# Kernel optimization log

Hardware: AMD Instinct MI355X
Metric: run time of the kernel (lower is better)

The kernel has to match this reference:

```python
import jax, jax.numpy as jnp
import numpy as np

B, L, DIM = 8, 2048, 768
EXPAND, D_STATE, D_CONV = 2, 16, 4
D_INNER = EXPAND * DIM           # 1536
DT_RANK = (DIM + 15) // 16       # 48
EPS = 1e-5


def setup_inputs() -> dict:
    key = jax.random.key(0)
    ks = jax.random.split(key, 8)
    s = lambda k, shape, scale=0.02: jax.random.normal(k, shape, jnp.float32) * scale
    x = jax.random.normal(ks[0], (B, L, DIM), jnp.float32)
    mask = jax.random.randint(ks[1], (B, L), 0, 2).astype(jnp.int32)
    return {
        "x": x,
        "mask": mask,
        "ln_g": jnp.ones((DIM,), jnp.float32),
        "ln_b": jnp.zeros((DIM,), jnp.float32),
        "W_in": s(ks[2], (2 * D_INNER, DIM)),
        "conv_w": s(ks[3], (D_INNER, 1, D_CONV), 0.1),
        "conv_b": jnp.zeros((D_INNER,), jnp.float32),
        "W_xp": s(ks[4], (DT_RANK + 2 * D_STATE, D_INNER)),
        "W_dt": s(ks[5], (D_INNER, DT_RANK), 0.1),
        "b_dt": jnp.full((D_INNER,), -4.6, jnp.float32),  # softplus(b) ~ 0.01 (standard dt init)
        "A_log": jnp.log(jnp.broadcast_to(jnp.arange(1.0, D_STATE + 1.0, dtype=jnp.float32), (D_INNER, D_STATE))),
        "Dp": jnp.ones((D_INNER,), jnp.float32),
        "W_out": s(ks[6], (DIM, D_INNER)),
    }


def _mamba(xn, W_in, conv_w, conv_b, W_xp, W_dt, b_dt, A_log, Dp, W_out):
    # in_proj then split into ssm branch and gate z
    xz = xn @ W_in.T                             # (B, L, 2*D_INNER)
    x_in, z = jnp.split(xz, 2, axis=-1)
    # depthwise causal conv1d + SiLU
    xc = jax.lax.conv_general_dilated(
        jnp.transpose(x_in, (0, 2, 1)), conv_w,
        window_strides=(1,), padding=[(D_CONV - 1, 0)],
        feature_group_count=D_INNER)             # (B, D_INNER, L)
    xc = jnp.transpose(jax.nn.silu(xc + conv_b[None, :, None]), (0, 2, 1))  # (B, L, D_INNER)
    # input-dependent dt, B, C
    xdbl = xc @ W_xp.T                           # (B, L, DT_RANK + 2*D_STATE)
    dt_in, Bm, Cm = jnp.split(xdbl, [DT_RANK, DT_RANK + D_STATE], axis=-1)
    dt = jax.nn.softplus(dt_in @ W_dt.T + b_dt)  # (B, L, D_INNER)
    A = -jnp.exp(A_log)                          # (D_INNER, D_STATE)

    def step(h, inp):
        dt_t, B_t, C_t, x_t = inp                # (B,D_INNER) (B,D_STATE) (B,D_STATE) (B,D_INNER)
        h = jnp.exp(dt_t[:, :, None] * A) * h + (dt_t * x_t)[:, :, None] * B_t[:, None, :]
        y = jnp.einsum('bds,bs->bd', h, C_t)
        return h, y

    h0 = jnp.zeros((B, D_INNER, D_STATE), xn.dtype)
    tm = lambda a: jnp.swapaxes(a, 0, 1)         # time-major for scan
    _, ys = jax.lax.scan(step, h0, (tm(dt), tm(Bm), tm(Cm), tm(xc)))
    y = jnp.swapaxes(ys, 0, 1) + xc * Dp         # skip term D*x
    y = y * jax.nn.silu(z)                       # gate
    return y @ W_out.T


def reference(x, mask, ln_g, ln_b, W_in, conv_w, conv_b, W_xp, W_dt, b_dt, A_log, Dp, W_out):
    mf = mask[..., None].astype(x.dtype)         # (B, L, 1)
    residual = x * mf
    mu = jnp.mean(x, -1, keepdims=True)
    var = jnp.mean((x - mu) ** 2, -1, keepdims=True)
    xn = (x - mu) * jax.lax.rsqrt(var + EPS) * ln_g + ln_b
    xn = xn * mf
    y = _mamba(xn, W_in, conv_w, conv_b, W_xp, W_dt, b_dt, A_log, Dp, W_out)
    # dropout is identity in eval mode
    return residual + y * mf
```

## Files before the change

kernel.cpp:

```cpp
#include <hip/hip_runtime.h>
#include <math.h>

#define Bn 8
#define Ln 2048
#define DIMn 768
#define DIN 1536
#define DSTATE 16
#define DTRANK 48
#define XPN 80
#define NR (Bn*Ln)
#define CH 128
#define NCH (Ln/CH)
#define NDG 6

typedef unsigned short bf16_t;
typedef __attribute__((ext_vector_type(8))) short short8;
typedef __attribute__((ext_vector_type(4))) float f32x4;
typedef __attribute__((ext_vector_type(4))) unsigned short u16x4;

__device__ __forceinline__ float sigf(float v){
    float e = __builtin_amdgcn_exp2f(v * -1.44269504f);
    return __builtin_amdgcn_rcpf(1.0f + e);
}
__device__ __forceinline__ float bf2f(unsigned short u){
    return __uint_as_float(((unsigned int)u) << 16);
}
__device__ __forceinline__ unsigned short f2bf(float f){
    unsigned int x = __float_as_uint(f);
    unsigned int r = (x + 0x7FFFu + ((x >> 16) & 1u)) >> 16;
    return (unsigned short)r;
}

__device__ __forceinline__ void async_ld16(const bf16_t* g, bf16_t* l) {
    __builtin_amdgcn_global_load_lds(
        (const __attribute__((address_space(1))) unsigned int*)g,
        (__attribute__((address_space(3))) unsigned int*)l,
        16, 0, 0);
}

#define ASM_BAR()   __builtin_amdgcn_s_barrier()
#define ASM_VM(N)   asm volatile("s_waitcnt vmcnt(" #N ")" ::: "memory")

__global__ __launch_bounds__(256) void f2bf_kernel(
    const float* __restrict__ in, bf16_t* __restrict__ out, int n)
{
    int i = blockIdx.x*256 + threadIdx.x;
    if (i < n) out[i] = f2bf(in[i]);
}
__global__ __launch_bounds__(256) void padxp_kernel(
    const float* __restrict__ W, bf16_t* __restrict__ out)
{
    int i = blockIdx.x*256 + threadIdx.x;
    int row = i / DIN, col = i % DIN;
    out[i] = (row < XPN) ? f2bf(W[row*DIN + col]) : 0;
}
__global__ __launch_bounds__(256) void paddt_kernel(
    const float* __restrict__ W, bf16_t* __restrict__ out)
{
    int i = blockIdx.x*256 + threadIdx.x;
    int row = i >> 6, col = i & 63;
    out[i] = (col < DTRANK) ? f2bf(W[row*DTRANK + col]) : 0;
}

__global__ __launch_bounds__(256) void ln_kernel(
    const float* __restrict__ x, const int* __restrict__ mask,
    const float* __restrict__ g, const float* __restrict__ bta,
    bf16_t* __restrict__ xn)
{
    int row = blockIdx.x;
    int t = threadIdx.x;
    const float* xr = x + (size_t)row * DIMn;
    float v0 = xr[t], v1 = xr[t+256], v2 = xr[t+512];
    float s  = v0+v1+v2;
    float sq = v0*v0+v1*v1+v2*v2;
    #pragma unroll
    for (int off = 32; off; off >>= 1) {
        s  += __shfl_down(s,  off, 64);
        sq += __shfl_down(sq, off, 64);
    }
    __shared__ float ls[4], lq[4];
    int wave = t >> 6, lane = t & 63;
    if (lane == 0) { ls[wave] = s; lq[wave] = sq; }
    __syncthreads();
    s  = ls[0]+ls[1]+ls[2]+ls[3];
    sq = lq[0]+lq[1]+lq[2]+lq[3];
    float mu  = s * (1.0f/DIMn);
    float var = sq * (1.0f/DIMn) - mu*mu;
    float rstd = rsqrtf(var + 1e-5f);
    float mf = (float)mask[row];
    bf16_t* o = xn + (size_t)row * DIMn;
    o[t]     = f2bf(((v0-mu)*rstd*g[t]     + bta[t])     * mf);
    o[t+256] = f2bf(((v1-mu)*rstd*g[t+256] + bta[t+256]) * mf);
    o[t+512] = f2bf(((v2-mu)*rstd*g[t+512] + bta[t+512]) * mf);
}

template<int EPI, typename TC>
__global__ __launch_bounds__(256) void mfma_gemm(
    const bf16_t* __restrict__ A, int lda,
    const bf16_t* __restrict__ W, int ldw,
    TC* __restrict__ C, int ldc, int K, int Nb,
    const float* __restrict__ bias,
    const float* __restrict__ resid, const int* __restrict__ mask)
{
    __shared__ __align__(16) bf16_t Als[8*512];
    __shared__ __align__(16) bf16_t Bls[8*512];
    int tid  = threadIdx.x;
    int wave = tid >> 6, lane = tid & 63;
    int mblk = blockIdx.y*128, nblk = blockIdx.x*128;
    int lr16 = lane & 15, kq = lane >> 4;
    int wr = wave >> 1, wc = wave & 1;
    f32x4 acc[4][4] = {};

    for (int k0 = 0; k0 < K; k0 += 32) {
        #pragma unroll
        for (int q = 0; q < 4; q++) {
            int id = wave*4 + q;
            if (id < 8) {
                const bf16_t* g = A + (size_t)(mblk + id*16 + lr16)*lda + k0 + kq*8;
                async_ld16(g, Als + id*512);
            } else {
                const bf16_t* g = W + (size_t)(nblk + (id-8)*16 + lr16)*ldw + k0 + kq*8;
                async_ld16(g, Bls + (id-8)*512);
            }
        }
        __syncthreads();
        short8 a[4], b[4];
        #pragma unroll
        for (int i = 0; i < 4; i++)
            a[i] = *(const short8*)(Als + (wr*4+i)*512 + lane*8);
        #pragma unroll
        for (int i = 0; i < 4; i++)
            b[i] = *(const short8*)(Bls + (wc*4+i)*512 + lane*8);
        #pragma unroll
        for (int mt = 0; mt < 4; mt++)
            #pragma unroll
            for (int nt = 0; nt < 4; nt++)
                acc[mt][nt] = __builtin_amdgcn_mfma_f32_16x16x32_bf16(
                    a[mt], b[nt], acc[mt][nt], 0, 0, 0);
        __syncthreads();
    }

    int m0 = mblk + wr*64, n0 = nblk + wc*64;
    int rb = kq*4;
    if constexpr (EPI == 3) {
        #pragma unroll
        for (int mt = 0; mt < 4; mt++) {
            #pragma unroll
            for (int nt = 0; nt < 4; nt++) {
                int colc = n0 + nt*16 + lr16;
                int rowb = m0 + mt*16 + rb;
                float bb = bias[colc];
                u16x4 o;
                #pragma unroll
                for (int r = 0; r < 4; r++) {
                    float u = acc[mt][nt][r] + bb;
                    float e = __builtin_amdgcn_exp2f(-fabsf(u) * 1.44269504f);
                    float sp = fmaxf(u, 0.f)
                             + 0.69314718f * __builtin_amdgcn_logf(1.0f + e);
                    o[r] = f2bf(sp);
                }
                *(u16x4*)((bf16_t*)C + (size_t)colc*ldc + rowb) = o;
            }
        }
    } else {
        #pragma unroll
        for (int mt = 0; mt < 4; mt++) {
            #pragma unroll
            for (int nt = 0; nt < 4; nt++) {
                int col = n0 + nt*16 + lr16;
                if (col >= Nb) continue;
                #pragma unroll
                for (int r = 0; r < 4; r++) {
                    int row = m0 + mt*16 + rb + r;
                    float v = acc[mt][nt][r];
                    C[(size_t)row*ldc + col] = f2bf(v);
                }
            }
        }
    }
}

#define BK2 32
#define RING 4
template<int EPI, typename TC>
__global__ __launch_bounds__(512, 2) void gemm256(
    const bf16_t* __restrict__ A, int lda,
    const bf16_t* __restrict__ W, int ldw,
    TC* __restrict__ C, int ldc, int K, int NXB,
    const float* __restrict__ resid, const int* __restrict__ mask)
{
    __shared__ __align__(16) bf16_t Als[RING][16][512];
    __shared__ __align__(16) bf16_t Bls[RING][16][512];

    int tid  = threadIdx.x;
    int w    = tid >> 6, lane = tid & 63;
    int lr16 = lane & 15, kq = lane >> 4;
    int wm   = w >> 2, wn = w & 3;
    int lane8 = lane * 8;

    int cpx  = gridDim.x >> 3;
    int bid  = blockIdx.x;
    int tile = (bid & 7) * cpx + (bid >> 3);
    int bn = tile % NXB, bm = tile / NXB;
    int mblk = bm * 256, nblk = bn * 256;

    int NT = K / BK2;

    const bf16_t* Arow0 = A + (size_t)(mblk + w*16     + lr16) * lda + kq*8;
    const bf16_t* Arow1 = A + (size_t)(mblk + (8+w)*16 + lr16) * lda + kq*8;
    const bf16_t* Wrow0 = W + (size_t)(nblk + w*16     + lr16) * ldw + kq*8;
    const bf16_t* Wrow1 = W + (size_t)(nblk + (8+w)*16 + lr16) * ldw + kq*8;

    f32x4 acc[8][4] = {};

    #pragma unroll
    for (int p = 0; p < 3; p++) {
        async_ld16(Arow0 + p*BK2, &Als[p][w][0]);
        async_ld16(Arow1 + p*BK2, &Als[p][8+w][0]);
        async_ld16(Wrow0 + p*BK2, &Bls[p][w][0]);
        async_ld16(Wrow1 + p*BK2, &Bls[p][8+w][0]);
    }
    ASM_VM(8);
    ASM_BAR();

    int s = 0;
    for (int t = 0; t < NT; ++t) {
        int ns = (s + 3) & 3;
        int t3 = t + 3;
        short8 a[8], b[4];
        #pragma unroll
        for (int i = 0; i < 8; i++)
            a[i] = *(const short8*)(&Als[s][wm*8 + i][lane8]);
        #pragma unroll
        for (int j = 0; j < 4; j++)
            b[j] = *(const short8*)(&Bls[s][wn*4 + j][lane8]);
        if (t3 < NT) {
            async_ld16(Arow0 + t3*BK2, &Als[ns][w][0]);
            async_ld16(Arow1 + t3*BK2, &Als[ns][8+w][0]);
            async_ld16(Wrow0 + t3*BK2, &Bls[ns][w][0]);
            async_ld16(Wrow1 + t3*BK2, &Bls[ns][8+w][0]);
        }
        __builtin_amdgcn_s_setprio(1);
        #pragma unroll
        for (int i = 0; i < 8; i++)
            #pragma unroll
            for (int j = 0; j < 4; j++)
                acc[i][j] = __builtin_amdgcn_mfma_f32_16x16x32_bf16(
                    b[j], a[i], acc[i][j], 0, 0, 0);
        __builtin_amdgcn_s_setprio(0);
        if (t + 1 < NT) {
            int rem = NT - 2 - t;
            if (rem >= 2)      { ASM_VM(8); }
            else if (rem == 1) { ASM_VM(4); }
            else               { ASM_VM(0); }
            ASM_BAR();
        }
        s = (s + 1) & 3;
    }

    int row0 = mblk + wm*128, col0 = nblk + wn*64;
    int rb = kq*4;
    #pragma unroll
    for (int i = 0; i < 8; i++) {
        int row = row0 + i*16 + lr16;
        if constexpr (EPI == 2) {
            float mf = (float)mask[row];
            const float* rrow = resid + (size_t)row*ldc;
            float* crow = (float*)C + (size_t)row*ldc;
            #pragma unroll
            for (int j = 0; j < 4; j++) {
                int colb = col0 + j*16 + rb;
                float4 rv = *(const float4*)(rrow + colb);
                float4 o;
                o.x = mf*(rv.x + acc[i][j][0]);
                o.y = mf*(rv.y + acc[i][j][1]);
                o.z = mf*(rv.z + acc[i][j][2]);
                o.w = mf*(rv.w + acc[i][j][3]);
                *(float4*)(crow + colb) = o;
            }
        } else {
            bf16_t* crow = (bf16_t*)C + (size_t)row*ldc;
            #pragma unroll
            for (int j = 0; j < 4; j++) {
                int colb = col0 + j*16 + rb;
                u16x4 o;
                o[0] = f2bf(acc[i][j][0]);
                o[1] = f2bf(acc[i][j][1]);
                o[2] = f2bf(acc[i][j][2]);
                o[3] = f2bf(acc[i][j][3]);
                *(u16x4*)(crow + colb) = o;
            }
        }
    }
}

__global__ __launch_bounds__(256) void conv_silu_kernel(
    const bf16_t* __restrict__ xz,
    const float* __restrict__ cw,
    const float* __restrict__ cb,
    bf16_t* __restrict__ xc)
{
    int idx = blockIdx.x*256 + threadIdx.x;
    int dh = idx % (DIN/2);
    int r  = idx / (DIN/2);
    int l  = r % Ln;
    int d  = dh*2;
    float4 w0 = *(const float4*)(cw + d*4);
    float4 w1 = *(const float4*)(cw + d*4 + 4);
    float a0 = cb[d], a1 = cb[d+1];
    #pragma unroll
    for (int j = 0; j < 4; j++) {
        int ll = l - 3 + j;
        if (ll >= 0) {
            ushort2 v = *(const ushort2*)(xz + (size_t)(r-3+j)*(2*DIN) + d);
            a0 += bf2f(v.x) * ((const float*)&w0)[j];
            a1 += bf2f(v.y) * ((const float*)&w1)[j];
        }
    }
    ushort2 o; o.x = f2bf(a0*sigf(a0)); o.y = f2bf(a1*sigf(a1));
    *(ushort2*)(xc + (size_t)r*DIN + d) = o;
}


__global__ __launch_bounds__(256) void scan1_kernel(
    const bf16_t* __restrict__ dtb,
    const bf16_t* __restrict__ xcb,
    const bf16_t* __restrict__ xdbl,
    float* __restrict__ hend,
    float* __restrict__ sumdt)
{
    __shared__ float Bf[CH][20];

    int t   = threadIdx.x;
    int blk = blockIdx.x;
    int ch  = blk & (NCH-1);
    int grp = blk >> 4;
    int b   = grp / NDG, dg = grp % NDG;
    int cl  = t;
    int d   = dg*256 + cl;
    size_t rbase = (size_t)b*Ln + (size_t)ch*CH;

    {
        int r = t >> 1, p = t & 1;
        short8 v = *(const short8*)(xdbl + (rbase + r)*XPN + DTRANK + p*8);
        float4 f0, f1;
        f0.x = bf2f(((unsigned short*)&v)[0]); f0.y = bf2f(((unsigned short*)&v)[1]);
        f0.z = bf2f(((unsigned short*)&v)[2]); f0.w = bf2f(((unsigned short*)&v)[3]);
        f1.x = bf2f(((unsigned short*)&v)[4]); f1.y = bf2f(((unsigned short*)&v)[5]);
        f1.z = bf2f(((unsigned short*)&v)[6]); f1.w = bf2f(((unsigned short*)&v)[7]);
        *(float4*)&Bf[r][p*8]     = f0;
        *(float4*)&Bf[r][p*8 + 4] = f1;
    }
    __syncthreads();

    float h[16];
    #pragma unroll
    for (int j = 0; j < 16; j++) h[j] = 0.f;
    float sdt = 0.f;
    const bf16_t* dp = dtb + (size_t)d*NR + rbase;
    const bf16_t* xp = xcb + rbase*DIN + d;

    for (int ts8 = 0; ts8 < CH/8; ts8++) {
        short8 dt8 = *(const short8*)(dp + ts8*8);
        #pragma unroll
        for (int k = 0; k < 8; k++) {
            int ts = ts8*8 + k;
            float dtv = bf2f(((unsigned short*)&dt8)[k]);
            float xv  = bf2f(xp[(size_t)ts*DIN]);
            sdt += dtv;
            float u  = dtv * xv;
            float E1 = __builtin_amdgcn_exp2f(dtv * -1.44269504f);
            float E2 = E1*E1, E3 = E2*E1, E4 = E2*E2;
            float Eb = 1.f;
            #pragma unroll
            for (int q = 0; q < 4; q++) {
                float4 Bv = *(const float4*)&Bf[ts][q*4];
                h[4*q+0] = (Eb*E1)*h[4*q+0] + u*Bv.x;
                h[4*q+1] = (Eb*E2)*h[4*q+1] + u*Bv.y;
                h[4*q+2] = (Eb*E3)*h[4*q+2] + u*Bv.z;
                h[4*q+3] = (Eb*E4)*h[4*q+3] + u*Bv.w;
                Eb *= E4;
            }
        }
    }
    float* hb = hend + ((size_t)(grp*NCH + ch)*16)*256 + cl;
    #pragma unroll
    for (int j = 0; j < 16; j++) hb[(size_t)j*256] = h[j];
    sumdt[(size_t)(grp*NCH + ch)*256 + cl] = sdt;
}

__global__ __launch_bounds__(256) void scan2_kernel(
    const bf16_t* __restrict__ dtb,
    const bf16_t* __restrict__ xcb,
    const bf16_t* __restrict__ xdbl,
    bf16_t* __restrict__ xz,
    const float* __restrict__ Dp,
    const float* __restrict__ hend,
    const float* __restrict__ sumdt)
{
    __shared__ float  Bf[CH][20];
    __shared__ float  Cf[CH][20];
    __shared__ bf16_t ybuf[32][264];

    int t   = threadIdx.x;
    int blk = blockIdx.x;
    int ch  = blk & (NCH-1);
    int grp = blk >> 4;
    int b   = grp / NDG, dg = grp % NDG;
    int cl  = t;
    int d   = dg*256 + cl;
    size_t rbase = (size_t)b*Ln + (size_t)ch*CH;
    float Dv = Dp[d];

    {
        int r = t >> 1, p = t & 1;
        const bf16_t* src = xdbl + (rbase + r)*XPN + DTRANK + p*16;
        short8 v0 = *(const short8*)src;
        short8 v1 = *(const short8*)(src + 8);
        float* dst = p ? &Cf[r][0] : &Bf[r][0];
        float4 f0, f1, f2, f3;
        f0.x = bf2f(((unsigned short*)&v0)[0]); f0.y = bf2f(((unsigned short*)&v0)[1]);
        f0.z = bf2f(((unsigned short*)&v0)[2]); f0.w = bf2f(((unsigned short*)&v0)[3]);
        f1.x = bf2f(((unsigned short*)&v0)[4]); f1.y = bf2f(((unsigned short*)&v0)[5]);
        f1.z = bf2f(((unsigned short*)&v0)[6]); f1.w = bf2f(((unsigned short*)&v0)[7]);
        f2.x = bf2f(((unsigned short*)&v1)[0]); f2.y = bf2f(((unsigned short*)&v1)[1]);
        f2.z = bf2f(((unsigned short*)&v1)[2]); f2.w = bf2f(((unsigned short*)&v1)[3]);
        f3.x = bf2f(((unsigned short*)&v1)[4]); f3.y = bf2f(((unsigned short*)&v1)[5]);
        f3.z = bf2f(((unsigned short*)&v1)[6]); f3.w = bf2f(((unsigned short*)&v1)[7]);
        *(float4*)(dst + 0)  = f0;
        *(float4*)(dst + 4)  = f1;
        *(float4*)(dst + 8)  = f2;
        *(float4*)(dst + 12) = f3;
    }

    float h[16];
    #pragma unroll
    for (int j = 0; j < 16; j++) h[j] = 0.f;
    for (int cc = 0; cc < ch; cc++) {
        float sd = sumdt[(size_t)(grp*NCH + cc)*256 + cl];
        const float* hb = hend + ((size_t)(grp*NCH + cc)*16)*256 + cl;
        float E1 = __builtin_amdgcn_exp2f(sd * -1.44269504f);
        float E2 = E1*E1, E3 = E2*E1, E4 = E2*E2;
        float Eb = 1.f;
        #pragma unroll
        for (int q = 0; q < 4; q++) {
            h[4*q+0] = (Eb*E1)*h[4*q+0] + hb[(size_t)(4*q+0)*256];
            h[4*q+1] = (Eb*E2)*h[4*q+1] + hb[(size_t)(4*q+1)*256];
            h[4*q+2] = (Eb*E3)*h[4*q+2] + hb[(size_t)(4*q+2)*256];
            h[4*q+3] = (Eb*E4)*h[4*q+3] + hb[(size_t)(4*q+3)*256];
            Eb *= E4;
        }
    }
    __syncthreads();

    const bf16_t* dp = dtb + (size_t)d*NR + rbase;
    const bf16_t* xp = xcb + rbase*DIN + d;

    for (int l0 = 0; l0 < CH; l0 += 32) {
        for (int q8 = 0; q8 < 4; q8++) {
            short8 dt8 = *(const short8*)(dp + l0 + q8*8);
            #pragma unroll
            for (int k = 0; k < 8; k++) {
                int ts2 = q8*8 + k;
                int ts  = l0 + ts2;
                float dtv = bf2f(((unsigned short*)&dt8)[k]);
                float xv  = bf2f(xp[(size_t)ts*DIN]);
                float u  = dtv * xv;
                float E1 = __builtin_amdgcn_exp2f(dtv * -1.44269504f);
                float E2 = E1*E1, E3 = E2*E1, E4 = E2*E2;
                float Eb = 1.f;
                float p  = 0.f;
                #pragma unroll
                for (int q = 0; q < 4; q++) {
                    float4 Bv = *(const float4*)&Bf[ts][q*4];
                    float4 Cv = *(const float4*)&Cf[ts][q*4];
                    h[4*q+0] = (Eb*E1)*h[4*q+0] + u*Bv.x;
                    h[4*q+1] = (Eb*E2)*h[4*q+1] + u*Bv.y;
                    h[4*q+2] = (Eb*E3)*h[4*q+2] + u*Bv.z;
                    h[4*q+3] = (Eb*E4)*h[4*q+3] + u*Bv.w;
                    p = fmaf(h[4*q+0], Cv.x, p);
                    p = fmaf(h[4*q+1], Cv.y, p);
                    p = fmaf(h[4*q+2], Cv.z, p);
                    p = fmaf(h[4*q+3], Cv.w, p);
                    Eb *= E4;
                }
                ybuf[ts2][cl] = f2bf(p + xv*Dv);
            }
        }
        __syncthreads();
        {
            int r2 = t >> 3, c0 = (t & 7)*32;
            size_t row = rbase + l0 + r2;
            const bf16_t* zrow = xz + row*(2*DIN) + DIN + dg*256 + c0;
            bf16_t*       orow = (bf16_t*)xz + row*(2*DIN) + dg*256 + c0;
            #pragma unroll
            for (int k = 0; k < 4; k++) {
                short8 zv8 = *(const short8*)(zrow + k*8);
                short8 yv8 = *(const short8*)&ybuf[r2][c0 + k*8];
                short8 o;
                #pragma unroll
                for (int j = 0; j < 8; j++) {
                    float zv = bf2f(((unsigned short*)&zv8)[j]);
                    float yv = bf2f(((unsigned short*)&yv8)[j]);
                    ((unsigned short*)&o)[j] = f2bf(yv * zv * sigf(zv));
                }
                *(short8*)(orow + k*8) = o;
            }
        }
        __syncthreads();
    }
}

extern "C" void kernel_launch(void* const* d_in, const int* in_sizes, int n_in,
                              void* d_out, int out_size, void* d_ws, size_t ws_size,
                              hipStream_t stream) {
    const float* x      = (const float*)d_in[0];
    const int*   mask   = (const int*)  d_in[1];
    const float* ln_g   = (const float*)d_in[2];
    const float* ln_b   = (const float*)d_in[3];
    const float* W_in   = (const float*)d_in[4];
    const float* conv_w = (const float*)d_in[5];
    const float* conv_b = (const float*)d_in[6];
    const float* W_xp   = (const float*)d_in[7];
    const float* W_dt   = (const float*)d_in[8];
    const float* b_dt   = (const float*)d_in[9];
    const float* Dp     = (const float*)d_in[11];
    const float* W_out  = (const float*)d_in[12];
    float* out = (float*)d_out;

    char* wsb = (char*)d_ws;
    size_t off = 0;
    bf16_t* xz    = (bf16_t*)(wsb + off); off += (size_t)NR*3072*2;
    bf16_t* xc    = (bf16_t*)(wsb + off); off += (size_t)NR*DIN*2;
    bf16_t* xdbl  = (bf16_t*)(wsb + off); off += (size_t)NR*XPN*2;
    char*   xnbR  = (wsb + off);          off += (size_t)NR*DIMn*2;
    bf16_t* Winb  = (bf16_t*)(wsb + off); off += (size_t)(2*DIN)*DIMn*2;
    bf16_t* Woutb = (bf16_t*)(wsb + off); off += (size_t)DIMn*DIN*2;

    bf16_t* xnb   = (bf16_t*)xnbR;
    float*  hend  = (float*)xnbR;
    float*  sumdt = hend + (size_t)48*16*16*256;
    bf16_t* Wxpb  = (bf16_t*)(sumdt + (size_t)48*16*256);
    bf16_t* Wdtb  = Wxpb + (size_t)128*DIN;

    bf16_t* dtb;
    if (ws_size >= off + (size_t)DIN*NR*2) {
        dtb = (bf16_t*)(wsb + off);
    } else {
        dtb = (bf16_t*)d_out;
    }

    f2bf_kernel<<<(2*DIN*DIMn + 255)/256, 256, 0, stream>>>(W_in,  Winb,  2*DIN*DIMn);
    f2bf_kernel<<<(DIMn*DIN  + 255)/256, 256, 0, stream>>>(W_out, Woutb, DIMn*DIN);

    ln_kernel<<<NR, 256, 0, stream>>>(x, mask, ln_g, ln_b, xnb);

    gemm256<0, bf16_t><<<(3072/256)*(NR/256), 512, 0, stream>>>(
        xnb, DIMn, Winb, DIMn, xz, 2*DIN, DIMn, 3072/256, nullptr, nullptr);

    padxp_kernel<<<(128*DIN + 255)/256, 256, 0, stream>>>(W_xp, Wxpb);
    paddt_kernel<<<(DIN*64  + 255)/256, 256, 0, stream>>>(W_dt, Wdtb);

    conv_silu_kernel<<<(NR*DIN/2)/256, 256, 0, stream>>>(xz, conv_w, conv_b, xc);

    mfma_gemm<0, bf16_t><<<dim3(1, NR/128), 256, 0, stream>>>(
        xc, DIN, Wxpb, DIN, xdbl, XPN, DIN, XPN, nullptr, nullptr, nullptr);

    mfma_gemm<3, bf16_t><<<dim3(DIN/128, NR/128), 256, 0, stream>>>(
        xdbl, XPN, Wdtb, 64, dtb, NR, 64, DIN, b_dt, nullptr, nullptr);

    scan1_kernel<<<Bn*NDG*NCH, 256, 0, stream>>>(dtb, xc, xdbl, hend, sumdt);

    scan2_kernel<<<Bn*NDG*NCH, 256, 0, stream>>>(dtb, xc, xdbl, xz, Dp, hend, sumdt);

    gemm256<2, float><<<(DIMn/256)*(NR/256), 512, 0, stream>>>(
        xz, 2*DIN, Woutb, DIN, out, DIMn, DIN, DIMn/256, x, mask);
}
```

Before: 593.4 us.

## Roll conv window across rows and use 64-row tiles for x_proj GEMM

The depthwise conv now has each thread handle 8 channels over 16 consecutive rows. It keeps the last three inputs in registers, so each input row is loaded once instead of four times, and it uses 16-byte vector loads and stores. The skinny x_proj GEMM (N=80) switches to a new kernel with 64-row M tiles and a 3-stage async LDS ring. This doubles the number of blocks, to improve occupancy across CUs on a GEMM that only has one column block. The trade-off is fewer conv blocks, each running a serial 16-row loop.

```diff
diff --git a/kernel.cpp b/kernel.cpp
--- a/kernel.cpp
+++ b/kernel.cpp
@@ -180,6 +180,84 @@
     }
 }
 
+__global__ __launch_bounds__(256) void mfma_gemm64(
+    const bf16_t* __restrict__ A, int lda,
+    const bf16_t* __restrict__ W, int ldw,
+    bf16_t* __restrict__ C, int ldc, int K, int Nb)
+{
+    __shared__ __align__(16) bf16_t Als[3][4*512];
+    __shared__ __align__(16) bf16_t Bls[3][8*512];
+    int tid  = threadIdx.x;
+    int wave = tid >> 6, lane = tid & 63;
+    int mblk = blockIdx.y*64, nblk = blockIdx.x*128;
+    int lr16 = lane & 15, kq = lane >> 4;
+    int wr = wave >> 1, wc = wave & 1;
+    f32x4 acc[2][4] = {};
+    int NT = K / 32;
+
+    auto stage = [&](int sl, int k0) {
+        #pragma unroll
+        for (int q = 0; q < 3; q++) {
+            int id = wave*3 + q;
+            if (id < 4) {
+                const bf16_t* g = A + (size_t)(mblk + id*16 + lr16)*lda + k0 + kq*8;
+                async_ld16(g, &Als[sl][id*512]);
+            } else {
+                const bf16_t* g = W + (size_t)(nblk + (id-4)*16 + lr16)*ldw + k0 + kq*8;
+                async_ld16(g, &Bls[sl][(id-4)*512]);
+            }
+        }
+    };
+
+    stage(0, 0);
+    stage(1, 32);
+    ASM_VM(3);
+    ASM_BAR();
+
+    int s = 0;
+    for (int t = 0; t < NT; ++t) {
+        short8 a[2], b[4];
+        #pragma unroll
+        for (int i = 0; i < 2; i++)
+            a[i] = *(const short8*)(&Als[s][(wr*2+i)*512 + lane*8]);
+        #pragma unroll
+        for (int j = 0; j < 4; j++)
+            b[j] = *(const short8*)(&Bls[s][(wc*4+j)*512 + lane*8]);
+        int ns = s + 2; if (ns >= 3) ns -= 3;
+        if (t + 2 < NT) stage(ns, (t+2)*32);
+        __builtin_amdgcn_s_setprio(1);
+        #pragma unroll
+        for (int i = 0; i < 2; i++)
+            #pragma unroll
+            for (int j = 0; j < 4; j++)
+                acc[i][j] = __builtin_amdgcn_mfma_f32_16x16x32_bf16(
+                    a[i], b[j], acc[i][j], 0, 0, 0);
+        __builtin_amdgcn_s_setprio(0);
+        if (t + 1 < NT) {
+            if (t + 2 < NT) { ASM_VM(3); }
+            else            { ASM_VM(0); }
+            ASM_BAR();
+        }
+        s = s + 1; if (s >= 3) s -= 3;
+    }
+
+    int m0 = mblk + wr*32, n0 = nblk + wc*64;
+    int rb = kq*4;
+    #pragma unroll
+    for (int mt = 0; mt < 2; mt++) {
+        #pragma unroll
+        for (int nt = 0; nt < 4; nt++) {
+            int col = n0 + nt*16 + lr16;
+            if (col >= Nb) continue;
+            #pragma unroll
+            for (int r = 0; r < 4; r++) {
+                int row = m0 + mt*16 + rb + r;
+                C[(size_t)row*ldc + col] = f2bf(acc[mt][nt][r]);
+            }
+        }
+    }
+}
+
 #define BK2 32
 #define RING 4
 template<int EPI, typename TC>
@@ -294,31 +372,46 @@
     }
 }
 
-__global__ __launch_bounds__(256) void conv_silu_kernel(
+__global__ __launch_bounds__(192) void conv_roll_kernel(
     const bf16_t* __restrict__ xz,
     const float* __restrict__ cw,
     const float* __restrict__ cb,
     bf16_t* __restrict__ xc)
 {
-    int idx = blockIdx.x*256 + threadIdx.x;
-    int dh = idx % (DIN/2);
-    int r  = idx / (DIN/2);
-    int l  = r % Ln;
-    int d  = dh*2;
-    float4 w0 = *(const float4*)(cw + d*4);
-    float4 w1 = *(const float4*)(cw + d*4 + 4);
-    float a0 = cb[d], a1 = cb[d+1];
-    #pragma unroll
-    for (int j = 0; j < 4; j++) {
-        int ll = l - 3 + j;
-        if (ll >= 0) {
-            ushort2 v = *(const ushort2*)(xz + (size_t)(r-3+j)*(2*DIN) + d);
-            a0 += bf2f(v.x) * ((const float*)&w0)[j];
-            a1 += bf2f(v.y) * ((const float*)&w1)[j];
-        }
-    }
-    ushort2 o; o.x = f2bf(a0*sigf(a0)); o.y = f2bf(a1*sigf(a1));
-    *(ushort2*)(xc + (size_t)r*DIN + d) = o;
+    int t   = threadIdx.x;
+    int seg = blockIdx.x;
+    int d0  = t*8;
+    int l0  = (seg & 127) * 16;
+    size_t row0 = (size_t)seg * 16;
+
+    float4 w[8]; float bias[8];
+    #pragma unroll
+    for (int j = 0; j < 8; j++) {
+        w[j]    = *(const float4*)(cw + (d0+j)*4);
+        bias[j] = cb[d0+j];
+    }
+
+    short8 x1 = {}, x2 = {}, x3 = {};
+    if (l0 != 0) {
+        x1 = *(const short8*)(xz + (row0-1)*(2*DIN) + d0);
+        x2 = *(const short8*)(xz + (row0-2)*(2*DIN) + d0);
+        x3 = *(const short8*)(xz + (row0-3)*(2*DIN) + d0);
+    }
+    for (int r = 0; r < 16; r++) {
+        short8 x0 = *(const short8*)(xz + (row0+r)*(2*DIN) + d0);
+        short8 o;
+        #pragma unroll
+        for (int j = 0; j < 8; j++) {
+            float a = bias[j];
+            a = fmaf(bf2f(((unsigned short*)&x3)[j]), w[j].x, a);
+            a = fmaf(bf2f(((unsigned short*)&x2)[j]), w[j].y, a);
+            a = fmaf(bf2f(((unsigned short*)&x1)[j]), w[j].z, a);
+            a = fmaf(bf2f(((unsigned short*)&x0)[j]), w[j].w, a);
+            ((unsigned short*)&o)[j] = f2bf(a * sigf(a));
+        }
+        *(short8*)(xc + (row0+r)*DIN + d0) = o;
+        x3 = x2; x2 = x1; x1 = x0;
+    }
 }
 
 
@@ -561,10 +654,10 @@
     padxp_kernel<<<(128*DIN + 255)/256, 256, 0, stream>>>(W_xp, Wxpb);
     paddt_kernel<<<(DIN*64  + 255)/256, 256, 0, stream>>>(W_dt, Wdtb);
 
-    conv_silu_kernel<<<(NR*DIN/2)/256, 256, 0, stream>>>(xz, conv_w, conv_b, xc);
-
-    mfma_gemm<0, bf16_t><<<dim3(1, NR/128), 256, 0, stream>>>(
-        xc, DIN, Wxpb, DIN, xdbl, XPN, DIN, XPN, nullptr, nullptr, nullptr);
+    conv_roll_kernel<<<NR/16, 192, 0, stream>>>(xz, conv_w, conv_b, xc);
+
+    mfma_gemm64<<<dim3(1, NR/64), 256, 0, stream>>>(
+        xc, DIN, Wxpb, DIN, xdbl, XPN, DIN, XPN);
 
     mfma_gemm<3, bf16_t><<<dim3(DIN/128, NR/128), 256, 0, stream>>>(
         xdbl, XPN, Wdtb, 64, dtb, NR, 64, DIN, b_dt, nullptr, nullptr);
```

After: 513.4 us. -13.5%, faster.
